# Kernel tuning notes

Hardware: AMD Instinct MI355X
Metric: run time of the kernel (lower is better)

The kernel has to match this reference:

```python
import jax, jax.numpy as jnp
import numpy as np

# --- dims (match init_kwargs) ---
B, IN_DIM, OUT_DIM, CAUSES_DIM = 4096, 512, 4096, 256
POOL = 2
N_STEPS = 10
GAMMA = 0.1
LR = 0.001  # fixed lr inside _IstaStep
S = int(np.sqrt(OUT_DIM))   # 64: side of the square code map
SP = S // POOL              # 32: pooled side
POOLED_DIM = SP * SP        # 1024: second dim of V (pool path)


def setup_inputs() -> dict:
    key = jax.random.key(0)
    k1, k2, k3 = jax.random.split(key, 3)
    inputs = jax.random.normal(k1, (B, IN_DIM), jnp.float32)
    limit = float(np.sqrt(6.0 / (OUT_DIM + IN_DIM)))  # glorot_uniform for W
    W = jax.random.uniform(k2, (OUT_DIM, IN_DIM), jnp.float32, -limit, limit)
    # pool_flag=True -> V ~ U(0, 1) with shape (causes_dim, pooled_dim)
    V = jax.random.uniform(k3, (CAUSES_DIM, POOLED_DIM), jnp.float32, 0.0, 1.0)
    return {"inputs": inputs, "W": W, "V": V}


def _soft_threshold(x, t):
    # _proxOp: max(x - t, 0) + min(x + t, 0)
    return jnp.maximum(x - t, 0.0) + jnp.minimum(x + t, 0.0)


def reference(inputs, W, V):
    Bn = inputs.shape[0]
    x0 = jnp.zeros((Bn, OUT_DIM), inputs.dtype)
    u0 = jnp.full((Bn, CAUSES_DIM), 0.1, inputs.dtype)   # zeros + 0.1
    rec0 = jnp.zeros((Bn, IN_DIM), inputs.dtype)

    def step(carry, _):
        x, u, _rec = carry
        outputs = x @ W                                   # [B, IN_DIM], linear activation
        # NOTE: original uses (1 + exp(-z)) * 0.5 (not a true sigmoid) — keep faithful
        causes = (1.0 + jnp.exp(-(u @ V))) * 0.5          # [B, POOLED_DIM]
        # nearest-neighbor upsample of the pooled cause map back to the code map
        causes_up = jnp.repeat(
            jnp.repeat(causes.reshape(Bn, SP, SP), POOL, axis=1), POOL, axis=2
        ).reshape(Bn, OUT_DIM)                            # [B, OUT_DIM]
        # T.grad(sum((inputs - x@W)^2), x) = 2 * (x@W - inputs) @ W.T
        grad_x = 2.0 * (outputs - inputs) @ W.T           # [B, OUT_DIM]
        # prior=0 in _get_output, so the _proxInnov branch is dead code
        x_new = jax.lax.stop_gradient(                    # disconnected_grad
            _soft_threshold(x - LR * grad_x, LR * GAMMA * causes_up))
        # 2x2 max pool over the square code map
        x_pool = x_new.reshape(Bn, SP, POOL, SP, POOL).max(axis=(2, 4)).reshape(Bn, POOLED_DIM)
        # T.grad(sum(causes(u) * x_pool * gamma), u): d causes/dz = -0.5*exp(-z)
        dcauses = -0.5 * jnp.exp(-(u @ V))                # [B, POOLED_DIM]
        grad_u = (dcauses * x_pool * GAMMA) @ V.T         # [B, CAUSES_DIM]
        u_new = jax.lax.stop_gradient(
            _soft_threshold(u - LR * grad_u, LR * GAMMA / 10.0))
        return (x_new, u_new, outputs), None

    (x, u, rec), _ = jax.lax.scan(step, (x0, u0, rec0), None, length=N_STEPS)
    # return_mode='rec': reconstruction computed in the last step (from x_{T-1})
    return rec
```

## Files before the change

### kernel.cpp

```cpp
#include <hip/hip_runtime.h>
#include <math.h>


#define NB 4096
#define IN_DIM 512
#define OUT_DIM 4096
#define CAUSES_DIM 256
#define POOLED_DIM 1024

typedef __attribute__((ext_vector_type(8))) short short8;
typedef __attribute__((ext_vector_type(4))) float f32x4;

static constexpr float LR = 0.001f;
static constexpr float GAMMA = 0.1f;

enum { EP_R = 0, EP_OUT, EP_UUP };

__device__ __forceinline__ float softthr(float v, float t) {
    return fmaxf(v - t, 0.0f) + fminf(v + t, 0.0f);
}
__device__ __forceinline__ unsigned short f2bf(float f) {
    unsigned int u = __builtin_bit_cast(unsigned int, f);
    u = (u + 0x7fffu + ((u >> 16) & 1u)) >> 16;
    return (unsigned short)u;
}
__device__ __forceinline__ float bf2f(unsigned short h) {
    return __builtin_bit_cast(float, (unsigned int)h << 16);
}
__device__ __forceinline__ void gload_lds16(const unsigned short* g, unsigned short* l) {
    __builtin_amdgcn_global_load_lds(
        (const __attribute__((address_space(1))) void*)g,
        (__attribute__((address_space(3))) void*)l, 16, 0, 0);
}

template<int ROWS, int K>
__device__ __forceinline__ void stage_tile(const unsigned short* __restrict__ g,
                                           unsigned short* l, int row0, int k0, int t)
{
#pragma unroll
    for (int j = 0; j < ROWS / 32; j++) {
        const int idx = j * 256 + t;
        const int row = idx >> 3;
        const int sl  = (idx & 7) ^ (row & 7);
        gload_lds16(g + (size_t)(row0 + row) * K + k0 + sl * 8,
                    l + (size_t)(idx & ~63) * 8);
    }
}

template<int BM, int BN, int K>
__device__ __forceinline__ void kloop3(unsigned short* lds,
    const unsigned short* __restrict__ A, const unsigned short* __restrict__ B,
    int m0, int n0, f32x4 (&acc)[BM / 32][BN / 32])
{
    constexpr int FM = BM / 32, FN = BN / 32;
    constexpr int NK = K / 64, ST = (BM + BN) * 64, L = (BM + BN) / 32;
    static_assert(NK >= 3, "pipeline needs >=3 K-tiles");
    const int t = threadIdx.x;
    const int lane = t & 63, wid = t >> 6;
    const int l15 = lane & 15, l7 = lane & 7, g = lane >> 4;
    const int wm0 = (wid >> 1) * (BM / 2), wn0 = (wid & 1) * (BN / 2);

    auto stage = [&](int s, int b) {
        stage_tile<BM, K>(A, lds + b * ST, m0, s * 64, t);
        stage_tile<BN, K>(B, lds + b * ST + BM * 64, n0, s * 64, t);
    };
    auto comp = [&](int b) {
        const unsigned short* As = lds + b * ST;
        const unsigned short* Bs = lds + b * ST + BM * 64;
#pragma unroll
        for (int ks = 0; ks < 2; ks++) {
            const int so = (((ks * 4) + g) ^ l7) * 8;
            short8 af[FM], bfv[FN];
#pragma unroll
            for (int fi = 0; fi < FM; fi++)
                af[fi] = *(const short8*)&As[(wm0 + fi * 16 + l15) * 64 + so];
#pragma unroll
            for (int fj = 0; fj < FN; fj++)
                bfv[fj] = *(const short8*)&Bs[(wn0 + fj * 16 + l15) * 64 + so];
#pragma unroll
            for (int fi = 0; fi < FM; fi++)
#pragma unroll
                for (int fj = 0; fj < FN; fj++)
                    acc[fi][fj] = __builtin_amdgcn_mfma_f32_16x16x32_bf16(
                        af[fi], bfv[fj], acc[fi][fj], 0, 0, 0);
        }
    };

    stage(0, 0); stage(1, 1); stage(2, 2);
    int b = 0;
#pragma unroll 1
    for (int i = 0; i < NK - 2; ++i) {
        asm volatile("s_waitcnt vmcnt(%0)" :: "n"(2 * L) : "memory");
        __builtin_amdgcn_s_barrier();
        comp(b);
        __builtin_amdgcn_s_barrier();
        if (i + 3 < NK) stage(i + 3, b);
        b = (b == 2) ? 0 : b + 1;
    }
    asm volatile("s_waitcnt vmcnt(%0)" :: "n"(L) : "memory");
    __builtin_amdgcn_s_barrier();
    comp(b);
    b = (b == 2) ? 0 : b + 1;
    asm volatile("s_waitcnt vmcnt(0)" ::: "memory");
    __builtin_amdgcn_s_barrier();
    comp(b);
}

template<int BM, int BN, int K>
__device__ __forceinline__ void kloop2(unsigned short* lds,
    const unsigned short* __restrict__ A, const unsigned short* __restrict__ B,
    int m0, int n0, f32x4 (&acc)[BM / 32][BN / 32])
{
    constexpr int FM = BM / 32, FN = BN / 32;
    constexpr int NK = K / 64, ST = (BM + BN) * 64, L = (BM + BN) / 32;
    static_assert(NK >= 2, "pipeline needs >=2 K-tiles");
    const int t = threadIdx.x;
    const int lane = t & 63, wid = t >> 6;
    const int l15 = lane & 15, l7 = lane & 7, g = lane >> 4;
    const int wm0 = (wid >> 1) * (BM / 2), wn0 = (wid & 1) * (BN / 2);

    auto stage = [&](int s, int b) {
        stage_tile<BM, K>(A, lds + b * ST, m0, s * 64, t);
        stage_tile<BN, K>(B, lds + b * ST + BM * 64, n0, s * 64, t);
    };
    auto comp = [&](int b) {
        const unsigned short* As = lds + b * ST;
        const unsigned short* Bs = lds + b * ST + BM * 64;
#pragma unroll
        for (int ks = 0; ks < 2; ks++) {
            const int so = (((ks * 4) + g) ^ l7) * 8;
            short8 af[FM], bfv[FN];
#pragma unroll
            for (int fi = 0; fi < FM; fi++)
                af[fi] = *(const short8*)&As[(wm0 + fi * 16 + l15) * 64 + so];
#pragma unroll
            for (int fj = 0; fj < FN; fj++)
                bfv[fj] = *(const short8*)&Bs[(wn0 + fj * 16 + l15) * 64 + so];
#pragma unroll
            for (int fi = 0; fi < FM; fi++)
#pragma unroll
                for (int fj = 0; fj < FN; fj++)
                    acc[fi][fj] = __builtin_amdgcn_mfma_f32_16x16x32_bf16(
                        af[fi], bfv[fj], acc[fi][fj], 0, 0, 0);
        }
    };

    stage(0, 0); stage(1, 1);
    int b = 0;
#pragma unroll 1
    for (int i = 0; i < NK - 1; ++i) {
        asm volatile("s_waitcnt vmcnt(%0)" :: "n"(L) : "memory");
        __builtin_amdgcn_s_barrier();
        comp(b);
        __builtin_amdgcn_s_barrier();
        if (i + 2 < NK) stage(i + 2, b);
        b ^= 1;
    }
    asm volatile("s_waitcnt vmcnt(0)" ::: "memory");
    __builtin_amdgcn_s_barrier();
    comp(b);
}

template<int BM, int BN, int N, int K, int EP>
__device__ void gemm_core(unsigned short* lds, int m0, int n0,
                          const unsigned short* __restrict__ A,
                          const unsigned short* __restrict__ B,
                          const float* __restrict__ auxf,
                          void* __restrict__ out0, void* __restrict__ out1)
{
    constexpr int FM = BM / 32, FN = BN / 32;
    const int t = threadIdx.x, lane = t & 63, wid = t >> 6;
    const int l15 = lane & 15, g = lane >> 4;
    const int wm0 = (wid >> 1) * (BM / 2), wn0 = (wid & 1) * (BN / 2);

    f32x4 acc[FM][FN];
#pragma unroll
    for (int fi = 0; fi < FM; fi++)
#pragma unroll
        for (int fj = 0; fj < FN; fj++) acc[fi][fj] = (f32x4){0.f, 0.f, 0.f, 0.f};

    kloop3<BM, BN, K>(lds, A, B, m0, n0, acc);

#pragma unroll
    for (int fi = 0; fi < FM; fi++) {
#pragma unroll
        for (int fj = 0; fj < FN; fj++) {
#pragma unroll
            for (int r = 0; r < 4; r++) {
                const int row = m0 + wm0 + fi * 16 + g * 4 + r;
                const int col = n0 + wn0 + fj * 16 + l15;
                const float v = acc[fi][fj][r];
                if (EP == EP_R) {
                    ((unsigned short*)out0)[(size_t)row * N + col] =
                        f2bf(v - auxf[(size_t)row * N + col]);
                } else if (EP == EP_OUT) {
                    ((float*)out0)[(size_t)row * N + col] = v;
                } else {
                    float* up = (float*)out0;
                    const size_t idx = (size_t)row * CAUSES_DIM + col;
                    const float uv = softthr(up[idx] - LR * v, LR * GAMMA * 0.1f);
                    up[idx] = uv;
                    ((unsigned short*)out1)[idx] = f2bf(uv);
                }
            }
        }
    }
}

template<bool FIRST, bool POOLF>
__global__ __launch_bounds__(256)
void xupc_kernel(const unsigned short* __restrict__ Rbf,
                 const unsigned short* __restrict__ Wbf,
                 const unsigned short* __restrict__ ubf,
                 const unsigned short* __restrict__ VTbf,
                 unsigned short* __restrict__ xbf,
                 unsigned short* __restrict__ gbf)
{
    constexpr int BM = 128, BN = 128;
    __shared__ unsigned short lds[2 * (BM + BN) * 64 + 8192];
    unsigned* czdc = (unsigned*)(lds + 2 * (BM + BN) * 64);
    unsigned short* xs = lds;

    const int t = threadIdx.x, lane = t & 63, wid = t >> 6;
    const int l15 = lane & 15, g = lane >> 4;
    const int xcd = blockIdx.x & 7, l = blockIdx.x >> 3;
    const int g2 = l >> 5, r2 = l & 31;
    const int bm = g2 * 8 + (r2 >> 2), bn = xcd * 4 + (r2 & 3);
    const int m0 = bm * BM, n0 = bn * BN;
    const int wm0 = (wid >> 1) * 64, wn0 = (wid & 1) * 64;

    f32x4 acc[4][4];
#pragma unroll
    for (int fi = 0; fi < 4; fi++)
#pragma unroll
        for (int fj = 0; fj < 4; fj++) acc[fi][fj] = (f32x4){0.f, 0.f, 0.f, 0.f};
    kloop2<128, 128, IN_DIM>(lds, Rbf, Wbf, m0, n0, acc);
    __syncthreads();

    f32x4 zacc[4][1];
#pragma unroll
    for (int fi = 0; fi < 4; fi++) zacc[fi][0] = (f32x4){0.f, 0.f, 0.f, 0.f};
    kloop2<128, 32, CAUSES_DIM>(lds, ubf, VTbf, m0, bn * 32, zacc);

    {
        const int zc = (wid & 1) * 16 + l15;
#pragma unroll
        for (int fi = 0; fi < 4; fi++) {
#pragma unroll
            for (int r = 0; r < 4; r++) {
                const int zr = (wid >> 1) * 64 + fi * 16 + g * 4 + r;
                const float e = expf(-zacc[fi][0][r]);
                czdc[zr * 32 + zc] =
                    (unsigned)f2bf(0.5f + 0.5f * e) | ((unsigned)f2bf(-0.5f * e) << 16);
            }
        }
    }
    __syncthreads();

#pragma unroll
    for (int fi = 0; fi < 4; fi++) {
#pragma unroll
        for (int fj = 0; fj < 4; fj++) {
#pragma unroll
            for (int r = 0; r < 4; r++) {
                const int rloc = wm0 + fi * 16 + g * 4 + r;
                const int cloc = wn0 + fj * 16 + l15;
                const int pl = (cloc & 63) >> 1;
                const float cz = bf2f((unsigned short)(czdc[rloc * 32 + pl] & 0xffffu));
                const size_t idx = (size_t)(m0 + rloc) * OUT_DIM + n0 + cloc;
                const float xold = FIRST ? 0.0f : bf2f(xbf[idx]);
                const float xv = softthr(xold - 2.0f * LR * acc[fi][fj][r],
                                         LR * GAMMA * cz);
                const unsigned short xq = f2bf(xv);
                xbf[idx] = xq;
                if (POOLF) xs[rloc * 130 + cloc] = xq;
            }
        }
    }

    if (POOLF) {
        __syncthreads();
        const int p = t & 31;
        const int rbase = (t >> 5) * 16;
#pragma unroll
        for (int i = 0; i < 16; i++) {
            const int prow = rbase + i;
            const unsigned short* xr = &xs[prow * 130 + 2 * p];
            const float mx = fmaxf(fmaxf(bf2f(xr[0]), bf2f(xr[1])),
                                   fmaxf(bf2f(xr[64]), bf2f(xr[65])));
            const float dcv = bf2f((unsigned short)(czdc[prow * 32 + p] >> 16));
            gbf[(size_t)(m0 + prow) * POOLED_DIM + bn * 32 + p] = f2bf(dcv * mx * GAMMA);
        }
    }
}

__global__ __launch_bounds__(256)
void h_uup_r_kernel(const unsigned short* __restrict__ gbf,
                    const unsigned short* __restrict__ Vbf,
                    float* __restrict__ u, unsigned short* __restrict__ ubf,
                    const unsigned short* __restrict__ xbf,
                    const unsigned short* __restrict__ WTbf,
                    const float* __restrict__ inputs,
                    unsigned short* __restrict__ Rbf)
{
    __shared__ unsigned short lds[3 * (128 + 64) * 64];
    if (blockIdx.x < 256) {
        const int bid = blockIdx.x;
        const int xcd = bid & 7, l = bid >> 3;
        const int bm = xcd * 4 + (l >> 3);
        const int bn = l & 7;
        gemm_core<128, 64, IN_DIM, OUT_DIM, EP_R>(
            lds, bm * 128, bn * 64, xbf, WTbf, inputs, Rbf, nullptr);
    } else {
        const int bid = blockIdx.x - 256;
        gemm_core<64, 64, CAUSES_DIM, POOLED_DIM, EP_UUP>(
            lds, (bid >> 2) * 64, (bid & 3) * 64, gbf, Vbf, nullptr, u, ubf);
    }
}

__global__ __launch_bounds__(256)
void out_kernel(const unsigned short* __restrict__ xbf,
                const unsigned short* __restrict__ WTbf,
                float* __restrict__ out)
{
    __shared__ unsigned short lds[3 * (128 + 64) * 64];
    const int bid = blockIdx.x;
    const int xcd = bid & 7, l = bid >> 3;
    const int bm = xcd * 4 + (l >> 3);
    const int bn = l & 7;
    gemm_core<128, 64, IN_DIM, OUT_DIM, EP_OUT>(
        lds, bm * 128, bn * 64, xbf, WTbf, nullptr, out, nullptr);
}

__global__ __launch_bounds__(256)
void prep_k(const float* __restrict__ in, unsigned short* __restrict__ direct,
            unsigned short* __restrict__ transp, int R, int C)
{
    __shared__ float tile[32][33];
    const int bx = blockIdx.x * 32, by = blockIdx.y * 32;
    const int tx = threadIdx.x % 32, ty = threadIdx.x / 32;
#pragma unroll
    for (int i = 0; i < 32; i += 8) {
        const float v = in[(size_t)(by + ty + i) * C + bx + tx];
        tile[ty + i][tx] = v;
        direct[(size_t)(by + ty + i) * C + bx + tx] = f2bf(v);
    }
    __syncthreads();
#pragma unroll
    for (int i = 0; i < 32; i += 8)
        transp[(size_t)(bx + ty + i) * R + by + tx] = f2bf(tile[tx][ty + i]);
}

__global__ void negcast_k(const float* __restrict__ in, unsigned short* __restrict__ out,
                          int n4)
{
    const int i = blockIdx.x * 256 + threadIdx.x;
    if (i >= n4) return;
    float4 v = ((const float4*)in)[i];
    union { unsigned short s[4]; unsigned long long u; } p;
    p.s[0] = f2bf(-v.x); p.s[1] = f2bf(-v.y); p.s[2] = f2bf(-v.z); p.s[3] = f2bf(-v.w);
    ((unsigned long long*)out)[i] = p.u;
}

__global__ void fill_u_k(float* __restrict__ u, unsigned short* __restrict__ ubf, int n) {
    const int i = blockIdx.x * 256 + threadIdx.x;
    if (i >= n) return;
    u[i] = 0.1f;
    ubf[i] = f2bf(0.1f);
}

extern "C" void kernel_launch(void* const* d_in, const int* in_sizes, int n_in,
                              void* d_out, int out_size, void* d_ws, size_t ws_size,
                              hipStream_t stream)
{
    const float* inputs = (const float*)d_in[0];
    const float* W      = (const float*)d_in[1];
    const float* V      = (const float*)d_in[2];
    float* out = (float*)d_out;

    char* w = (char*)d_ws;
    unsigned short* xbf  = (unsigned short*)w; w += (size_t)NB * OUT_DIM * 2;
    unsigned short* Rbf  = (unsigned short*)w; w += (size_t)NB * IN_DIM * 2;
    unsigned short* gbf  = (unsigned short*)w; w += (size_t)NB * POOLED_DIM * 2;
    float*          u    = (float*)w;          w += (size_t)NB * CAUSES_DIM * 4;
    unsigned short* ubf  = (unsigned short*)w; w += (size_t)NB * CAUSES_DIM * 2;
    unsigned short* Wbf  = (unsigned short*)w; w += (size_t)OUT_DIM * IN_DIM * 2;
    unsigned short* WTbf = (unsigned short*)w; w += (size_t)OUT_DIM * IN_DIM * 2;
    unsigned short* Vbf  = (unsigned short*)w; w += (size_t)CAUSES_DIM * POOLED_DIM * 2;
    unsigned short* VTbf = (unsigned short*)w;

    prep_k<<<dim3(IN_DIM / 32, OUT_DIM / 32), 256, 0, stream>>>(W, Wbf, WTbf, OUT_DIM, IN_DIM);
    prep_k<<<dim3(POOLED_DIM / 32, CAUSES_DIM / 32), 256, 0, stream>>>(V, Vbf, VTbf, CAUSES_DIM, POOLED_DIM);
    fill_u_k<<<NB * CAUSES_DIM / 256, 256, 0, stream>>>(u, ubf, NB * CAUSES_DIM);
    negcast_k<<<NB * IN_DIM / 4 / 256, 256, 0, stream>>>(inputs, Rbf, NB * IN_DIM / 4);

    xupc_kernel<true, true><<<1024, 256, 0, stream>>>(Rbf, Wbf, ubf, VTbf, xbf, gbf);
    h_uup_r_kernel<<<512, 256, 0, stream>>>(gbf, Vbf, u, ubf, xbf, WTbf, inputs, Rbf);
    for (int t = 1; t < 8; t++) {
        xupc_kernel<false, true><<<1024, 256, 0, stream>>>(Rbf, Wbf, ubf, VTbf, xbf, gbf);
        h_uup_r_kernel<<<512, 256, 0, stream>>>(gbf, Vbf, u, ubf, xbf, WTbf, inputs, Rbf);
    }
    xupc_kernel<false, false><<<1024, 256, 0, stream>>>(Rbf, Wbf, ubf, VTbf, xbf, gbf);
    out_kernel<<<256, 256, 0, stream>>>(xbf, WTbf, out);
}
```

Before: 737.1 us.

## Read LDS fragments into registers before issuing next-stage loads and MFMAs

Each K-tile's LDS fragments for both k-substeps are now read into registers first, followed by a wait on LDS reads and a barrier. Only then does the loop issue the next global-to-LDS stage and run all MFMAs. This lets the buffer be refilled while the matrix math is still running, and the epilogue iterations are folded into the loop. MFMAs run at raised wave priority via s_setprio. The change doubles fragment register usage, which may reduce occupancy or cause spills.

Measured after the change: 682.4 us. 7.4% less time.

```diff
diff --git a/kernel.cpp b/kernel.cpp
--- a/kernel.cpp
+++ b/kernel.cpp
@@ -64,46 +64,54 @@
         stage_tile<BM, K>(A, lds + b * ST, m0, s * 64, t);
         stage_tile<BN, K>(B, lds + b * ST + BM * 64, n0, s * 64, t);
     };
-    auto comp = [&](int b) {
+
+    short8 af[2][FM], bfv[2][FN];
+    auto readfrags = [&](int b) {
         const unsigned short* As = lds + b * ST;
         const unsigned short* Bs = lds + b * ST + BM * 64;
 #pragma unroll
         for (int ks = 0; ks < 2; ks++) {
             const int so = (((ks * 4) + g) ^ l7) * 8;
-            short8 af[FM], bfv[FN];
 #pragma unroll
             for (int fi = 0; fi < FM; fi++)
-                af[fi] = *(const short8*)&As[(wm0 + fi * 16 + l15) * 64 + so];
+                af[ks][fi] = *(const short8*)&As[(wm0 + fi * 16 + l15) * 64 + so];
 #pragma unroll
             for (int fj = 0; fj < FN; fj++)
-                bfv[fj] = *(const short8*)&Bs[(wn0 + fj * 16 + l15) * 64 + so];
+                bfv[ks][fj] = *(const short8*)&Bs[(wn0 + fj * 16 + l15) * 64 + so];
+        }
+    };
+    auto mfma_all = [&]() {
+        __builtin_amdgcn_s_setprio(1);
+#pragma unroll
+        for (int ks = 0; ks < 2; ks++)
 #pragma unroll
             for (int fi = 0; fi < FM; fi++)
 #pragma unroll
                 for (int fj = 0; fj < FN; fj++)
                     acc[fi][fj] = __builtin_amdgcn_mfma_f32_16x16x32_bf16(
-                        af[fi], bfv[fj], acc[fi][fj], 0, 0, 0);
-        }
+                        af[ks][fi], bfv[ks][fj], acc[fi][fj], 0, 0, 0);
+        __builtin_amdgcn_s_setprio(0);
     };
 
     stage(0, 0); stage(1, 1); stage(2, 2);
     int b = 0;
 #pragma unroll 1
-    for (int i = 0; i < NK - 2; ++i) {
-        asm volatile("s_waitcnt vmcnt(%0)" :: "n"(2 * L) : "memory");
+    for (int i = 0; i < NK; ++i) {
+        if (i < NK - 2)
+            asm volatile("s_waitcnt vmcnt(%0)" :: "n"(2 * L) : "memory");
+        else if (i == NK - 2)
+            asm volatile("s_waitcnt vmcnt(%0)" :: "n"(L) : "memory");
+        else
+            asm volatile("s_waitcnt vmcnt(0)" ::: "memory");
         __builtin_amdgcn_s_barrier();
-        comp(b);
+        readfrags(b);
+        asm volatile("s_waitcnt lgkmcnt(0)" ::: "memory");
+        __builtin_amdgcn_sched_barrier(0);
         __builtin_amdgcn_s_barrier();
         if (i + 3 < NK) stage(i + 3, b);
+        mfma_all();
         b = (b == 2) ? 0 : b + 1;
     }
-    asm volatile("s_waitcnt vmcnt(%0)" :: "n"(L) : "memory");
-    __builtin_amdgcn_s_barrier();
-    comp(b);
-    b = (b == 2) ? 0 : b + 1;
-    asm volatile("s_waitcnt vmcnt(0)" ::: "memory");
-    __builtin_amdgcn_s_barrier();
-    comp(b);
 }
 
 template<int BM, int BN, int K>
@@ -123,42 +131,52 @@
         stage_tile<BM, K>(A, lds + b * ST, m0, s * 64, t);
         stage_tile<BN, K>(B, lds + b * ST + BM * 64, n0, s * 64, t);
     };
-    auto comp = [&](int b) {
+
+    short8 af[2][FM], bfv[2][FN];
+    auto readfrags = [&](int b) {
         const unsigned short* As = lds + b * ST;
         const unsigned short* Bs = lds + b * ST + BM * 64;
 #pragma unroll
         for (int ks = 0; ks < 2; ks++) {
             const int so = (((ks * 4) + g) ^ l7) * 8;
-            short8 af[FM], bfv[FN];
 #pragma unroll
             for (int fi = 0; fi < FM; fi++)
-                af[fi] = *(const short8*)&As[(wm0 + fi * 16 + l15) * 64 + so];
+                af[ks][fi] = *(const short8*)&As[(wm0 + fi * 16 + l15) * 64 + so];
 #pragma unroll
             for (int fj = 0; fj < FN; fj++)
-                bfv[fj] = *(const short8*)&Bs[(wn0 + fj * 16 + l15) * 64 + so];
+                bfv[ks][fj] = *(const short8*)&Bs[(wn0 + fj * 16 + l15) * 64 + so];
+        }
+    };
+    auto mfma_all = [&]() {
+        __builtin_amdgcn_s_setprio(1);
+#pragma unroll
+        for (int ks = 0; ks < 2; ks++)
 #pragma unroll
             for (int fi = 0; fi < FM; fi++)
 #pragma unroll
                 for (int fj = 0; fj < FN; fj++)
                     acc[fi][fj] = __builtin_amdgcn_mfma_f32_16x16x32_bf16(
-                        af[fi], bfv[fj], acc[fi][fj], 0, 0, 0);
-        }
+                        af[ks][fi], bfv[ks][fj], acc[fi][fj], 0, 0, 0);
+        __builtin_amdgcn_s_setprio(0);
     };
 
     stage(0, 0); stage(1, 1);
     int b = 0;
 #pragma unroll 1
-    for (int i = 0; i < NK - 1; ++i) {
-        asm volatile("s_waitcnt vmcnt(%0)" :: "n"(L) : "memory");
+    for (int i = 0; i < NK; ++i) {
+        if (i < NK - 1)
+            asm volatile("s_waitcnt vmcnt(%0)" :: "n"(L) : "memory");
+        else
+            asm volatile("s_waitcnt vmcnt(0)" ::: "memory");
         __builtin_amdgcn_s_barrier();
-        comp(b);
+        readfrags(b);
+        asm volatile("s_waitcnt lgkmcnt(0)" ::: "memory");
+        __builtin_amdgcn_sched_barrier(0);
         __builtin_amdgcn_s_barrier();
         if (i + 2 < NK) stage(i + 2, b);
+        mfma_all();
         b ^= 1;
     }
-    asm volatile("s_waitcnt vmcnt(0)" ::: "memory");
-    __builtin_amdgcn_s_barrier();
-    comp(b);
 }
 
 template<int BM, int BN, int N, int K, int EP>
```
